# Kernel tuning notes

Measured on AMD Instinct MI355X. Metric: run time of the kernel, lower is better.

Reference implementation:

```python
import jax, jax.numpy as jnp
import numpy as np

IN_F, OUT_F = 2048, 2048
IQ, OQ = IN_F // 4, OUT_F // 4
B, S = 4, 4096


def _xavier(key, shape):
    fan_out, fan_in = shape
    limit = float(np.sqrt(6.0 / (fan_in + fan_out)))
    return jax.random.uniform(key, shape, jnp.float32, -limit, limit)


def setup_inputs() -> dict:
    key = jax.random.key(0)
    kx, kr, ki, kj, kk = jax.random.split(key, 5)
    return {
        "x": jax.random.normal(kx, (B, S, IN_F), dtype=jnp.float32),
        "wr": _xavier(kr, (OQ, IQ)),
        "wi": _xavier(ki, (OQ, IQ)),
        "wj": _xavier(kj, (OQ, IQ)),
        "wk": _xavier(kk, (OQ, IQ)),
        "bias": jnp.zeros((OUT_F,), dtype=jnp.float32),
    }


def reference(x, wr, wi, wj, wk, bias):
    b, s, _ = x.shape
    iq = wr.shape[1]
    oq = wr.shape[0]
    # strided quaternion component extraction: x[..., c::4] -> (B*S, iq)
    xq = x.reshape(b * s, iq, 4)  # last-dim interleaved layout
    xr, xi, xj, xk = xq[..., 0], xq[..., 1], xq[..., 2], xq[..., 3]
    # small GEMMs against W^T (W is (oq, iq)); only the products actually used
    Ar = xr @ wr.T
    Br = xi @ wr.T
    Cr = xj @ wr.T
    Dr = xk @ wr.T
    Ai = xr @ wi.T
    Bi = xi @ wi.T
    Aj = xr @ wj.T
    Cj = xj @ wj.T
    Ak = xr @ wk.T
    Dk = xk @ wk.T
    # combine exactly as in the original module
    or_ = Ar - Bi - Cj - Dk
    oi_ = Br + Ai + Dk - Cj
    oj_ = Cr - Dk + Aj + Bi
    ok_ = Dr + Cj - Bi + Ak
    # interleaved scatter: out[:, c::4] = o<c>
    out = jnp.stack([or_, oi_, oj_, ok_], axis=-1).reshape(b, s, 4 * oq)
    return out + bias[None, None, :]
```

## Files before the change

### kernel.cpp

```cpp
#include <hip/hip_runtime.h>


typedef unsigned short u16;
typedef __bf16 bf16x8 __attribute__((ext_vector_type(8)));
typedef float f32x4 __attribute__((ext_vector_type(4)));

#define QM 16384
#define QN 2048
#define QK 2048

__device__ __forceinline__ u16 f2bf(float f) {
    union { float f; unsigned u; } v;
    v.f = f;
    unsigned r = v.u + 0x7FFFu + ((v.u >> 16) & 1u);
    return (u16)(r >> 16);
}

__device__ __forceinline__ void async_copy16(const u16* g, u16* l) {
    __builtin_amdgcn_global_load_lds(
        (const __attribute__((address_space(1))) void*)g,
        (__attribute__((address_space(3))) void*)l,
        16, 0, 0);
}

__global__ void prep_kernel(const float* __restrict__ x, u16* __restrict__ xb,
                            const float* __restrict__ wr, const float* __restrict__ wi,
                            const float* __restrict__ wj, const float* __restrict__ wk,
                            u16* __restrict__ wb) {
    const int b = blockIdx.x;
    if (b < 4096) {
        const int n4 = (QM * QK) / 4;
        for (int i = b * blockDim.x + threadIdx.x; i < n4; i += 4096 * blockDim.x) {
            float4 v = reinterpret_cast<const float4*>(x)[i];
            ushort4 o;
            o.x = f2bf(v.x); o.y = f2bf(v.y); o.z = f2bf(v.z); o.w = f2bf(v.w);
            reinterpret_cast<ushort4*>(xb)[i] = o;
        }
    } else {
        int i = (b - 4096) * blockDim.x + threadIdx.x;
        int n = i >> 9;
        int p = i & 511;
        int q = n >> 2, co = n & 3;
        int base = (q << 9) + p;
        float r  = wr[base], ii = wi[base], jj = wj[base], kk = wk[base];
        float e0, e1, e2, e3;
        if      (co == 0) { e0 = r;  e1 = -ii; e2 = -jj; e3 = -kk; }
        else if (co == 1) { e0 = ii; e1 = r;   e2 = -jj; e3 = kk;  }
        else if (co == 2) { e0 = jj; e1 = ii;  e2 = r;   e3 = -kk; }
        else              { e0 = kk; e1 = -ii; e2 = jj;  e3 = r;   }
        ushort4 o;
        o.x = f2bf(e0); o.y = f2bf(e1); o.z = f2bf(e2); o.w = f2bf(e3);
        reinterpret_cast<ushort4*>(wb)[(n << 9) + p] = o;
    }
}

__global__ __launch_bounds__(512, 2) void qgemm_kernel(const u16* __restrict__ A,
                                                       const u16* __restrict__ B,
                                                       const float* __restrict__ bias,
                                                       float* __restrict__ C) {
    __shared__ __align__(16) u16 L[81920];

    const int bid = blockIdx.x;
    const int swz = (bid & 7) * 64 + (bid >> 3);
    const int bm = swz >> 3;
    const int bn = swz & 7;

    const int tid = threadIdx.x;
    const int wid = tid >> 6, lane = tid & 63;
    const int wm = wid >> 2, wn = wid & 3;
    const int lr = lane & 15, lg = lane >> 4;

    const u16* Asrc = A + (size_t)bm * 256 * QK;
    const u16* Bsrc = B + (size_t)bn * 256 * QK;

    const int rA  = tid >> 3;
    const int clA = ((tid & 7) ^ (rA & 7)) << 3;
    const size_t soff = (size_t)rA * QK + clA;

    f32x4 acc[8][4];
#pragma unroll
    for (int i = 0; i < 8; ++i)
#pragma unroll
        for (int j = 0; j < 4; ++j)
            acc[i][j] = (f32x4){0.f, 0.f, 0.f, 0.f};

    auto stage = [&](const u16* src, int lbase, int k0) {
#pragma unroll
        for (int o = 0; o < 2; ++o)
            async_copy16(src + (size_t)(o * 64) * QK + k0 + soff,
                         &L[lbase + o * 4096 + wid * 512]);
    };

    auto rdA = [&](const u16* LA, int mf, int ks) -> bf16x8 {
        const int r = wm * 128 + mf * 16 + lr;
        const int c = ((ks * 4 + lg) ^ (r & 7)) << 3;
        return *(const bf16x8*)&LA[r * 64 + c];
    };
    auto rdB = [&](const u16* LB, int nf, int ks) -> bf16x8 {
        const int r = wn * 64 + nf * 16 + lr;
        const int c = ((ks * 4 + lg) ^ (r & 7)) << 3;
        return *(const bf16x8*)&LB[r * 64 + c];
    };

    auto doTile = [&](const int ab, const int bt, const int bt2, const int t)
        __attribute__((always_inline)) {
        const u16* LA = &L[ab * 16384];
        const u16* LB = &L[32768 + bt * 16384];
        const int tw1 = (t + 1) & 31, tw2 = (t + 2) & 31;
        const int oA = (ab ^ 1) * 16384;
        const int oB = 32768 + bt2 * 16384;

        bf16x8 a0[4], a1[4], b0[4], b1[4];

#pragma unroll
        for (int nf = 0; nf < 4; ++nf) b0[nf] = rdB(LB, nf, 0);
#pragma unroll
        for (int mf = 0; mf < 4; ++mf) a0[mf] = rdA(LA, mf, 0);
        stage(Asrc, oA, tw1 * 64);
#pragma unroll
        for (int mf = 0; mf < 4; ++mf)
#pragma unroll
            for (int nf = 0; nf < 4; ++nf)
                acc[mf][nf] = __builtin_amdgcn_mfma_f32_16x16x32_bf16(a0[mf], b0[nf], acc[mf][nf], 0, 0, 0);

#pragma unroll
        for (int mf = 0; mf < 4; ++mf) a1[mf] = rdA(LA, 4 + mf, 0);
#pragma unroll
        for (int nf = 0; nf < 4; ++nf) b1[nf] = rdB(LB, nf, 1);
        stage(Asrc + 128 * QK, oA + 8192, tw1 * 64);
#pragma unroll
        for (int mf = 0; mf < 4; ++mf)
#pragma unroll
            for (int nf = 0; nf < 4; ++nf)
                acc[4 + mf][nf] = __builtin_amdgcn_mfma_f32_16x16x32_bf16(a1[mf], b0[nf], acc[4 + mf][nf], 0, 0, 0);

#pragma unroll
        for (int mf = 0; mf < 4; ++mf) a0[mf] = rdA(LA, mf, 1);
        stage(Bsrc, oB, tw2 * 64);
#pragma unroll
        for (int mf = 0; mf < 4; ++mf)
#pragma unroll
            for (int nf = 0; nf < 4; ++nf)
                acc[mf][nf] = __builtin_amdgcn_mfma_f32_16x16x32_bf16(a0[mf], b1[nf], acc[mf][nf], 0, 0, 0);

#pragma unroll
        for (int mf = 0; mf < 4; ++mf) a1[mf] = rdA(LA, 4 + mf, 1);
        stage(Bsrc + 128 * QK, oB + 8192, tw2 * 64);
#pragma unroll
        for (int mf = 0; mf < 4; ++mf)
#pragma unroll
            for (int nf = 0; nf < 4; ++nf)
                acc[4 + mf][nf] = __builtin_amdgcn_mfma_f32_16x16x32_bf16(a1[mf], b1[nf], acc[4 + mf][nf], 0, 0, 0);

        asm volatile("s_waitcnt lgkmcnt(0) vmcnt(4)" ::: "memory");
        __builtin_amdgcn_s_barrier();
    };

    stage(Asrc,            0,             0);
    stage(Asrc + 128 * QK, 8192,          0);
    stage(Bsrc,            32768,             0);
    stage(Bsrc + 128 * QK, 32768 + 8192,      0);
    stage(Bsrc,            32768 + 16384,        64);
    stage(Bsrc + 128 * QK, 32768 + 16384 + 8192, 64);
    asm volatile("s_waitcnt vmcnt(4)" ::: "memory");
    __builtin_amdgcn_s_barrier();

    for (int t = 0; t < 30; t += 6) {
        doTile(0, 0, 2, t);
        doTile(1, 1, 0, t + 1);
        doTile(0, 2, 1, t + 2);
        doTile(1, 0, 2, t + 3);
        doTile(0, 1, 0, t + 4);
        doTile(1, 2, 1, t + 5);
    }
    doTile(0, 0, 2, 30);
    doTile(1, 1, 0, 31);

    const int colbase = bn * 256 + wn * 64;
    const int rowbase = bm * 256 + wm * 128;
    float bsv[4];
#pragma unroll
    for (int nf = 0; nf < 4; ++nf) bsv[nf] = bias[colbase + nf * 16 + lr];
    float* Cb = C + (size_t)rowbase * QN + colbase;
#pragma unroll
    for (int mf = 0; mf < 8; ++mf)
#pragma unroll
        for (int nf = 0; nf < 4; ++nf)
#pragma unroll
            for (int v = 0; v < 4; ++v)
                Cb[(size_t)(mf * 16 + lg * 4 + v) * QN + nf * 16 + lr] = acc[mf][nf][v] + bsv[nf];
}

extern "C" void kernel_launch(void* const* d_in, const int* in_sizes, int n_in,
                              void* d_out, int out_size, void* d_ws, size_t ws_size,
                              hipStream_t stream) {
    const float* x    = (const float*)d_in[0];
    const float* wr   = (const float*)d_in[1];
    const float* wi   = (const float*)d_in[2];
    const float* wj   = (const float*)d_in[3];
    const float* wk   = (const float*)d_in[4];
    const float* bias = (const float*)d_in[5];
    float* out = (float*)d_out;

    u16* xb = (u16*)d_ws;
    u16* wb = (u16*)((char*)d_ws + (size_t)QM * QK * 2);

    prep_kernel<<<8192, 256, 0, stream>>>(x, xb, wr, wi, wj, wk, wb);
    qgemm_kernel<<<512, 512, 0, stream>>>(xb, wb, bias, out);
}
```

Measured before the change: 159.1 us.

## Software-pipeline LDS fragment reads across tile barrier with register prefetch

Restructures the per-tile loop so the first A/B fragments of the next tile are read from LDS right after the barrier, while the last MFMA group of the current tile is still to be issued. Fragment reads for each MFMA group are also issued one group ahead. The aim is to hide LDS read latency behind matrix math instead of stalling at the start of each tile. The cost is more live vector registers (extra a2/a3 plus persistent a0/b0), which could hurt register allocation at 2 waves-per-SIMD launch bounds.

```diff
diff --git a/kernel.cpp b/kernel.cpp
--- a/kernel.cpp
+++ b/kernel.cpp
@@ -102,58 +102,64 @@
         return *(const bf16x8*)&LB[r * 64 + c];
     };
 
-    auto doTile = [&](const int ab, const int bt, const int bt2, const int t)
-        __attribute__((always_inline)) {
-        const u16* LA = &L[ab * 16384];
-        const u16* LB = &L[32768 + bt * 16384];
+    bf16x8 a0[4], b0[4];
+
+    auto doTile = [&](const int ab, const int bt, const int bt2,
+                      const int abn, const int btn, const int t,
+                      const bool preRead) __attribute__((always_inline)) {
+        const u16* LA  = &L[ab * 16384];
+        const u16* LB  = &L[32768 + bt * 16384];
+        const u16* LAn = &L[abn * 16384];
+        const u16* LBn = &L[32768 + btn * 16384];
         const int tw1 = (t + 1) & 31, tw2 = (t + 2) & 31;
-        const int oA = (ab ^ 1) * 16384;
+        const int oA = abn * 16384;
         const int oB = 32768 + bt2 * 16384;
 
-        bf16x8 a0[4], a1[4], b0[4], b1[4];
-
-#pragma unroll
-        for (int nf = 0; nf < 4; ++nf) b0[nf] = rdB(LB, nf, 0);
-#pragma unroll
-        for (int mf = 0; mf < 4; ++mf) a0[mf] = rdA(LA, mf, 0);
+        bf16x8 a1[4], b1[4], a2[4], a3[4];
+
         stage(Asrc, oA, tw1 * 64);
 #pragma unroll
+        for (int mf = 0; mf < 4; ++mf) a1[mf] = rdA(LA, 4 + mf, 0);
+#pragma unroll
         for (int mf = 0; mf < 4; ++mf)
 #pragma unroll
             for (int nf = 0; nf < 4; ++nf)
                 acc[mf][nf] = __builtin_amdgcn_mfma_f32_16x16x32_bf16(a0[mf], b0[nf], acc[mf][nf], 0, 0, 0);
 
-#pragma unroll
-        for (int mf = 0; mf < 4; ++mf) a1[mf] = rdA(LA, 4 + mf, 0);
+        stage(Asrc + 128 * QK, oA + 8192, tw1 * 64);
 #pragma unroll
         for (int nf = 0; nf < 4; ++nf) b1[nf] = rdB(LB, nf, 1);
-        stage(Asrc + 128 * QK, oA + 8192, tw1 * 64);
+#pragma unroll
+        for (int mf = 0; mf < 4; ++mf) a2[mf] = rdA(LA, mf, 1);
 #pragma unroll
         for (int mf = 0; mf < 4; ++mf)
 #pragma unroll
             for (int nf = 0; nf < 4; ++nf)
                 acc[4 + mf][nf] = __builtin_amdgcn_mfma_f32_16x16x32_bf16(a1[mf], b0[nf], acc[4 + mf][nf], 0, 0, 0);
 
-#pragma unroll
-        for (int mf = 0; mf < 4; ++mf) a0[mf] = rdA(LA, mf, 1);
         stage(Bsrc, oB, tw2 * 64);
 #pragma unroll
-        for (int mf = 0; mf < 4; ++mf)
-#pragma unroll
-            for (int nf = 0; nf < 4; ++nf)
-                acc[mf][nf] = __builtin_amdgcn_mfma_f32_16x16x32_bf16(a0[mf], b1[nf], acc[mf][nf], 0, 0, 0);
-
-#pragma unroll
-        for (int mf = 0; mf < 4; ++mf) a1[mf] = rdA(LA, 4 + mf, 1);
+        for (int mf = 0; mf < 4; ++mf) a3[mf] = rdA(LA, 4 + mf, 1);
+#pragma unroll
+        for (int mf = 0; mf < 4; ++mf)
+#pragma unroll
+            for (int nf = 0; nf < 4; ++nf)
+                acc[mf][nf] = __builtin_amdgcn_mfma_f32_16x16x32_bf16(a2[mf], b1[nf], acc[mf][nf], 0, 0, 0);
+
         stage(Bsrc + 128 * QK, oB + 8192, tw2 * 64);
-#pragma unroll
-        for (int mf = 0; mf < 4; ++mf)
-#pragma unroll
-            for (int nf = 0; nf < 4; ++nf)
-                acc[4 + mf][nf] = __builtin_amdgcn_mfma_f32_16x16x32_bf16(a1[mf], b1[nf], acc[4 + mf][nf], 0, 0, 0);
-
         asm volatile("s_waitcnt lgkmcnt(0) vmcnt(4)" ::: "memory");
         __builtin_amdgcn_s_barrier();
+        if (preRead) {
+#pragma unroll
+            for (int nf = 0; nf < 4; ++nf) b0[nf] = rdB(LBn, nf, 0);
+#pragma unroll
+            for (int mf = 0; mf < 4; ++mf) a0[mf] = rdA(LAn, mf, 0);
+        }
+#pragma unroll
+        for (int mf = 0; mf < 4; ++mf)
+#pragma unroll
+            for (int nf = 0; nf < 4; ++nf)
+                acc[4 + mf][nf] = __builtin_amdgcn_mfma_f32_16x16x32_bf16(a3[mf], b1[nf], acc[4 + mf][nf], 0, 0, 0);
     };
 
     stage(Asrc,            0,             0);
@@ -164,17 +170,21 @@
     stage(Bsrc + 128 * QK, 32768 + 16384 + 8192, 64);
     asm volatile("s_waitcnt vmcnt(4)" ::: "memory");
     __builtin_amdgcn_s_barrier();
+#pragma unroll
+    for (int nf = 0; nf < 4; ++nf) b0[nf] = rdB(&L[32768], nf, 0);
+#pragma unroll
+    for (int mf = 0; mf < 4; ++mf) a0[mf] = rdA(&L[0], mf, 0);
 
     for (int t = 0; t < 30; t += 6) {
-        doTile(0, 0, 2, t);
-        doTile(1, 1, 0, t + 1);
-        doTile(0, 2, 1, t + 2);
-        doTile(1, 0, 2, t + 3);
-        doTile(0, 1, 0, t + 4);
-        doTile(1, 2, 1, t + 5);
+        doTile(0, 0, 2, 1, 1, t,     true);
+        doTile(1, 1, 0, 0, 2, t + 1, true);
+        doTile(0, 2, 1, 1, 0, t + 2, true);
+        doTile(1, 0, 2, 0, 1, t + 3, true);
+        doTile(0, 1, 0, 1, 2, t + 4, true);
+        doTile(1, 2, 1, 0, 0, t + 5, true);
     }
-    doTile(0, 0, 2, 30);
-    doTile(1, 1, 0, 31);
+    doTile(0, 0, 2, 1, 1, 30, true);
+    doTile(1, 1, 0, 0, 2, 31, false);
 
     const int colbase = bn * 256 + wn * 64;
     const int rowbase = bm * 256 + wm * 128;
```

Measured after the change: 153.9 us, median of 2. 3.3% less time.
